# Kernel optimization log

Hardware: AMD Instinct MI355X
Metric: run time of the kernel (lower is better)

## Reference

```python
import jax, jax.numpy as jnp
import numpy as np

NUM_HEADS = 16


def setup_inputs() -> dict:
    key = jax.random.key(0)
    ks = jax.random.split(key, 5)
    B, S, E = 4, 2048, 1024
    scale = 1.0 / np.sqrt(E)
    return {
        "x": jax.random.normal(ks[0], (B, S, E), dtype=jnp.float32),
        "w_in": jax.random.normal(ks[1], (E, 3 * E), dtype=jnp.float32) * scale,
        "b_in": jax.random.normal(ks[2], (3 * E,), dtype=jnp.float32) * 0.02,
        "w_out": jax.random.normal(ks[3], (E, E), dtype=jnp.float32) * scale,
        "b_out": jax.random.normal(ks[4], (E,), dtype=jnp.float32) * 0.02,
    }


def reference(x, w_in, b_in, w_out, b_out):
    B, S, E = x.shape
    H = NUM_HEADS
    D = E // H  # head dim
    qkv = x @ w_in + b_in                      # [B,S,3E]
    q, k, v = jnp.split(qkv, 3, axis=-1)       # each [B,S,E]
    q = q.reshape(B, S, H, D)
    k = k.reshape(B, S, H, D)
    v = v.reshape(B, S, H, D)
    # scores scaled by 1/sqrt(D); note: original's causal masked_fill is a
    # no-op (not in-place), so attention is unmasked.
    scores = jnp.einsum("bqhd,bkhd->bhqk", q, k) / jnp.sqrt(jnp.float32(D))
    attn = jax.nn.softmax(scores, axis=-1)      # [B,H,S,S]
    out = jnp.einsum("bhqk,bkhd->bqhd", attn, v).reshape(B, S, E)
    return out @ w_out + b_out
```

## Files before the change

### kernel.cpp

```cpp
#include <hip/hip_runtime.h>
#include <math.h>

#define B_ 4
#define S_ 2048
#define E_ 1024
#define H_ 16
#define D_ 64
#define M_ (B_ * S_)

using f32x4  = __attribute__((ext_vector_type(4))) float;
using short8 = __attribute__((ext_vector_type(8))) short;
using half8  = __attribute__((ext_vector_type(8))) _Float16;
using ushort8_t = __attribute__((ext_vector_type(8))) unsigned short;

__device__ inline unsigned short f2h(float f) {
    _Float16 h = (_Float16)f;
    unsigned short u; __builtin_memcpy(&u, &h, 2); return u;
}
__device__ inline unsigned pk2h(float a, float b) {
    auto t = __builtin_amdgcn_cvt_pkrtz(a, b);
    unsigned u; __builtin_memcpy(&u, &t, 4); return u;
}
__device__ inline float ex2(float x) {
#if __has_builtin(__builtin_amdgcn_exp2f)
    return __builtin_amdgcn_exp2f(x);
#else
    return exp2f(x);
#endif
}
__device__ inline f32x4 mfma16(short8 a, short8 b, f32x4 c) {
    half8 ha, hb;
    __builtin_memcpy(&ha, &a, 16);
    __builtin_memcpy(&hb, &b, 16);
    return __builtin_amdgcn_mfma_f32_16x16x32_f16(ha, hb, c, 0, 0, 0);
}
__device__ inline void gload_lds16(const void* g, void* l) {
    __builtin_amdgcn_global_load_lds(
        (const __attribute__((address_space(1))) void*)g,
        (__attribute__((address_space(3))) void*)l, 16, 0, 0);
}

#define QSCALE 0.18033688f

__global__ __launch_bounds__(256)
void prep_kernel(const float* __restrict__ x,     unsigned short* __restrict__ xh,
                 const float* __restrict__ w_in,  unsigned short* __restrict__ wInTh,
                 const float* __restrict__ w_out, unsigned short* __restrict__ wOutTh)
{
    __shared__ float t[32][33];
    const int bid  = blockIdx.x;
    const int tidx = threadIdx.x;
    if (bid < (M_ * E_) / 1024) {
        const size_t i = ((size_t)bid * 256 + tidx) * 4;
        float4 v = *(const float4*)(x + i);
        ushort4 hh;
        hh.x = f2h(v.x); hh.y = f2h(v.y); hh.z = f2h(v.z); hh.w = f2h(v.w);
        *(ushort4*)(xh + i) = hh;
        return;
    }
    const float* W; unsigned short* T; int C, c0, r0;
    if (bid < 8192 + 3072) {
        const int t2 = bid - 8192;
        W = w_in;  T = wInTh;  C = 3 * E_;
        c0 = (t2 % 96) * 32;  r0 = (t2 / 96) * 32;
    } else {
        const int t2 = bid - 11264;
        W = w_out; T = wOutTh; C = E_;
        c0 = (t2 & 31) * 32;  r0 = (t2 >> 5) * 32;
    }
    const int tx = tidx & 31, ty = tidx >> 5;
    #pragma unroll
    for (int i = 0; i < 4; ++i)
        t[ty + 8 * i][tx] = W[(size_t)(r0 + ty + 8 * i) * C + c0 + tx];
    __syncthreads();
    #pragma unroll
    for (int i = 0; i < 4; ++i)
        T[(size_t)(c0 + ty + 8 * i) * E_ + r0 + tx] = f2h(t[tx][ty + 8 * i]);
}

template<int OUT_MODE>
__global__ __launch_bounds__(256)
void gemm_mfma_kernel(const unsigned short* __restrict__ Ah,
                      const unsigned short* __restrict__ Bt,
                      const float* __restrict__ bias,
                      float* __restrict__ Cf,
                      unsigned short* __restrict__ Ch,
                      int M, int N, int K)
{
    __shared__ unsigned short As[128][64];
    __shared__ unsigned short Bs[128][64];

    const int tid  = threadIdx.x;
    const int lane = tid & 63;
    const int wave = tid >> 6;
    const int wm = (wave >> 1) * 64, wn = (wave & 1) * 64;
    const int ln = lane & 15, qd = lane >> 4;
    const int m0 = blockIdx.x * 128, n0 = blockIdx.y * 128;

    f32x4 acc[4][4] = {};

    const int srow_l = lane >> 3;
    const int scol   = ((lane & 7) ^ srow_l) * 8;
    const int swz    = (ln & 7) * 8;

    for (int k0 = 0; k0 < K; k0 += 64) {
        #pragma unroll
        for (int c = 0; c < 4; ++c) {
            const int r = wave * 32 + c * 8;
            const size_t ga = (size_t)(m0 + r + srow_l) * K + k0 + scol;
            const size_t gb = (size_t)(n0 + r + srow_l) * K + k0 + scol;
            gload_lds16(Ah + ga, &As[r][0]);
            gload_lds16(Bt + gb, &Bs[r][0]);
        }
        __syncthreads();

        #pragma unroll
        for (int ks = 0; ks < 2; ++ks) {
            const int co = (ks * 32 + qd * 8) ^ swz;
            short8 aa[4], bb[4];
            #pragma unroll
            for (int mt = 0; mt < 4; ++mt)
                aa[mt] = *(const short8*)&As[wm + mt * 16 + ln][co];
            #pragma unroll
            for (int nt = 0; nt < 4; ++nt)
                bb[nt] = *(const short8*)&Bs[wn + nt * 16 + ln][co];
            __builtin_amdgcn_s_setprio(1);
            #pragma unroll
            for (int mt = 0; mt < 4; ++mt)
                #pragma unroll
                for (int nt = 0; nt < 4; ++nt)
                    acc[mt][nt] = mfma16(aa[mt], bb[nt], acc[mt][nt]);
            __builtin_amdgcn_s_setprio(0);
        }
        __syncthreads();
    }

    #pragma unroll
    for (int nt = 0; nt < 4; ++nt) {
        const int col = n0 + wn + nt * 16 + ln;
        const float bv = bias[col];
        const float scale = (OUT_MODE == 2 && col < E_) ? QSCALE : 1.0f;
        #pragma unroll
        for (int mt = 0; mt < 4; ++mt) {
            #pragma unroll
            for (int r = 0; r < 4; ++r) {
                const int row = m0 + wm + mt * 16 + qd * 4 + r;
                float f = acc[mt][nt][r] + bv;
                size_t idx = (size_t)row * N + col;
                if (OUT_MODE == 0) Cf[idx] = f;
                else               Ch[idx] = f2h(f * scale);
            }
        }
    }
}

__global__ __launch_bounds__(512)
void attn_mfma_kernel(const unsigned short* __restrict__ qkvh,
                      unsigned short* __restrict__ outh)
{
    constexpr int TQ = 256, TK = 64, LD = 64;
    __shared__ unsigned short Ksh[TK][LD];
    __shared__ unsigned short VthA[D_][LD];
    __shared__ unsigned short VthB[D_][LD];

    const int tid  = threadIdx.x;
    const int lane = tid & 63;
    const int wave = tid >> 6;
    const int ln = lane & 15, qd = lane >> 4;
    const int id   = blockIdx.x;
    const int g    = id & 63;
    const int qblk = id >> 6;
    const int h    = g & 15;
    const int b    = g >> 4;
    const int wq0 = wave * 32;
    const int swz = (ln & 7) * 8;

    short8 ones8;
    #pragma unroll
    for (int j = 0; j < 8; ++j) ones8[j] = (short)0x3C00;

    short8 qh[2][2];
    #pragma unroll
    for (int qt = 0; qt < 2; ++qt)
        #pragma unroll
        for (int ks = 0; ks < 2; ++ks) {
            size_t base = ((size_t)(b * S_ + qblk * TQ + wq0 + qt * 16 + ln)) * (3 * E_)
                        + h * 64 + ks * 32 + qd * 8;
            qh[qt][ks] = *(const short8*)(qkvh + base);
        }

    f32x4 o[4][2] = {};
    f32x4 ol[2]   = {};
    short8 pBp[2][2] = {};

    const int stid = tid & 255;
    const int krow = stid >> 2, kcol = (stid & 3) * 16;
    const int kswz = (krow & 7) * 8;
    const int vkey = (stid & 31) * 2, vdc = (stid >> 5) * 8;
    const int vslot = (vkey & 0x23) | ((vkey & 0x0C) << 1) | ((vkey & 0x10) >> 2);

    {
        ushort8_t z = {};
        *(ushort8_t*)(&VthB[0][0] + tid * 8) = z;
    }

    ushort8_t pk0 = {}, pk1 = {}, pv0 = {}, pv1 = {};
    if (wave < 4) {
        size_t gb = ((size_t)(b * S_ + krow)) * (3 * E_) + E_ + h * 64 + kcol;
        pk0 = *(const ushort8_t*)(qkvh + gb);
        pk1 = *(const ushort8_t*)(qkvh + gb + 8);
    } else {
        size_t vb0 = ((size_t)(b * S_ + vkey)) * (3 * E_) + 2 * E_ + h * 64 + vdc;
        pv0 = *(const ushort8_t*)(qkvh + vb0);
        pv1 = *(const ushort8_t*)(qkvh + vb0 + 3 * E_);
    }

    #define TILE_BODY(VW, VR, PREFETCH_KB, DO_PREFETCH)                        \
    {                                                                          \
        if (wave < 4) {                                                        \
            *(ushort8_t*)&Ksh[krow][kcol ^ kswz]       = pk0;                  \
            *(ushort8_t*)&Ksh[krow][(kcol + 8) ^ kswz] = pk1;                  \
        } else {                                                               \
            _Pragma("unroll")                                                  \
            for (int j = 0; j < 8; ++j)                                        \
                *(unsigned*)&VW[vdc + j][vslot ^ (j * 8)] =                    \
                    (unsigned)pv0[j] | ((unsigned)pv1[j] << 16);               \
        }                                                                      \
        __syncthreads();                                                       \
        if (DO_PREFETCH) {                                                     \
            if (wave < 4) {                                                    \
                size_t gb_ = ((size_t)(b * S_ + (PREFETCH_KB) + krow))         \
                           * (3 * E_) + E_ + h * 64 + kcol;                    \
                pk0 = *(const ushort8_t*)(qkvh + gb_);                         \
                pk1 = *(const ushort8_t*)(qkvh + gb_ + 8);                     \
            } else {                                                           \
                size_t vb_ = ((size_t)(b * S_ + (PREFETCH_KB) + vkey))         \
                           * (3 * E_) + 2 * E_ + h * 64 + vdc;                 \
                pv0 = *(const ushort8_t*)(qkvh + vb_);                         \
                pv1 = *(const ushort8_t*)(qkvh + vb_ + 3 * E_);                \
            }                                                                  \
        }                                                                      \
        f32x4 st[4][2] = {};                                                   \
        _Pragma("unroll")                                                      \
        for (int ks = 0; ks < 2; ++ks) {                                       \
            const int co = (ks * 32 + qd * 8) ^ swz;                           \
            short8 kh[4];                                                      \
            _Pragma("unroll")                                                  \
            for (int kt = 0; kt < 4; ++kt)                                     \
                kh[kt] = *(const short8*)&Ksh[kt * 16 + ln][co];               \
            __builtin_amdgcn_s_setprio(1);                                     \
            _Pragma("unroll")                                                  \
            for (int kt = 0; kt < 4; ++kt)                                     \
                _Pragma("unroll")                                              \
                for (int qt = 0; qt < 2; ++qt)                                 \
                    st[kt][qt] = mfma16(kh[kt], qh[qt][ks], st[kt][qt]);       \
            __builtin_amdgcn_s_setprio(0);                                     \
        }                                                                      \
                \
        _Pragma("unroll")                                                      \
        for (int ks = 0; ks < 2; ++ks) {                                       \
            const int co = (ks * 32 + qd * 8) ^ swz;                           \
            short8 vA[4];                                                      \
            _Pragma("unroll")                                                  \
            for (int dt = 0; dt < 4; ++dt)                                     \
                vA[dt] = *(const short8*)&VR[dt * 16 + ln][co];                \
            __builtin_amdgcn_s_setprio(1);                                     \
            _Pragma("unroll")                                                  \
            for (int dt = 0; dt < 4; ++dt)                                     \
                _Pragma("unroll")                                              \
                for (int qt = 0; qt < 2; ++qt)                                 \
                    o[dt][qt] = mfma16(vA[dt], pBp[ks][qt], o[dt][qt]);        \
            _Pragma("unroll")                                                  \
            for (int qt = 0; qt < 2; ++qt)                                     \
                ol[qt] = mfma16(ones8, pBp[ks][qt], ol[qt]);                   \
            __builtin_amdgcn_s_setprio(0);                                     \
        }                                                                      \
                             \
        _Pragma("unroll")                                                      \
        for (int qt = 0; qt < 2; ++qt)                                         \
            _Pragma("unroll")                                                  \
            for (int ks = 0; ks < 2; ++ks) {                                   \
                unsigned w_[4];                                                \
                w_[0] = pk2h(ex2(st[2 * ks][qt][0]), ex2(st[2 * ks][qt][1]));  \
                w_[1] = pk2h(ex2(st[2 * ks][qt][2]), ex2(st[2 * ks][qt][3]));  \
                w_[2] = pk2h(ex2(st[2 * ks + 1][qt][0]),                       \
                             ex2(st[2 * ks + 1][qt][1]));                      \
                w_[3] = pk2h(ex2(st[2 * ks + 1][qt][2]),                       \
                             ex2(st[2 * ks + 1][qt][3]));                      \
                __builtin_memcpy(&pBp[ks][qt], w_, 16);                        \
            }                                                                  \
        __syncthreads();                                                       \
    }

    for (int kb = 0; kb < S_; kb += 2 * TK) {
        TILE_BODY(VthA, VthB, kb + TK, true);
        TILE_BODY(VthB, VthA, kb + 2 * TK, (kb + 2 * TK < S_));
    }
    #undef TILE_BODY

    #pragma unroll
    for (int ks = 0; ks < 2; ++ks) {
        const int co = (ks * 32 + qd * 8) ^ swz;
        short8 vA[4];
        #pragma unroll
        for (int dt = 0; dt < 4; ++dt)
            vA[dt] = *(const short8*)&VthB[dt * 16 + ln][co];
        #pragma unroll
        for (int dt = 0; dt < 4; ++dt)
            #pragma unroll
            for (int qt = 0; qt < 2; ++qt)
                o[dt][qt] = mfma16(vA[dt], pBp[ks][qt], o[dt][qt]);
        #pragma unroll
        for (int qt = 0; qt < 2; ++qt)
            ol[qt] = mfma16(ones8, pBp[ks][qt], ol[qt]);
    }

    float inv[2];
    #pragma unroll
    for (int qt = 0; qt < 2; ++qt)
        inv[qt] = 1.0f / ol[qt][0];
    #pragma unroll
    for (int qt = 0; qt < 2; ++qt) {
        const int q = qblk * TQ + wq0 + qt * 16 + ln;
        #pragma unroll
        for (int dt = 0; dt < 4; ++dt) {
            size_t base = ((size_t)(b * S_ + q)) * E_ + h * 64 + dt * 16 + qd * 4;
            ushort4 hh;
            #pragma unroll
            for (int r = 0; r < 4; ++r)
                ((unsigned short*)&hh)[r] = f2h(o[dt][qt][r] * inv[qt]);
            *(ushort4*)(outh + base) = hh;
        }
    }
}

extern "C" void kernel_launch(void* const* d_in, const int* in_sizes, int n_in,
                              void* d_out, int out_size, void* d_ws, size_t ws_size,
                              hipStream_t stream)
{
    const float* x     = (const float*)d_in[0];
    const float* w_in  = (const float*)d_in[1];
    const float* b_in  = (const float*)d_in[2];
    const float* w_out = (const float*)d_in[3];
    const float* b_out = (const float*)d_in[4];
    float* outp = (float*)d_out;

    char* ws = (char*)d_ws;
    unsigned short* qkvh   = (unsigned short*)ws;
    unsigned short* attnh  = qkvh   + (size_t)M_ * 3 * E_;
    unsigned short* xh     = attnh  + (size_t)M_ * E_;
    unsigned short* wOutTh = xh     + (size_t)M_ * E_;
    unsigned short* wInTh  = attnh;

    prep_kernel<<<dim3(8192 + 3072 + 1024), 256, 0, stream>>>(
        x, xh, w_in, wInTh, w_out, wOutTh);

    gemm_mfma_kernel<2><<<dim3(M_ / 128, (3 * E_) / 128), 256, 0, stream>>>(
        xh, wInTh, b_in, nullptr, qkvh, M_, 3 * E_, E_);

    attn_mfma_kernel<<<dim3((S_ / 256) * H_ * B_), 512, 0, stream>>>(
        qkvh, attnh);

    gemm_mfma_kernel<0><<<dim3(M_ / 128, E_ / 128), 256, 0, stream>>>(
        attnh, wOutTh, b_out, outp, nullptr, M_, E_, E_);
}
```

Before: 267.8 us.

## Double-buffer LDS tiles in MFMA GEMM to overlap global loads with compute

The GEMM kernel now keeps two LDS buffers for the A and B tiles and issues the global-to-LDS loads for the next K tile before computing on the current one. Explicit vmcnt waits let the prefetch stay in flight while the current tile is consumed. This hides global load latency behind MFMA work in the QKV and output projections. In exchange, LDS use per block doubles to 64KB, which may lower occupancy, and correctness depends on the hand-written waitcnt counts matching the number of outstanding loads.

```diff
diff --git a/kernel.cpp b/kernel.cpp
--- a/kernel.cpp
+++ b/kernel.cpp
@@ -87,8 +87,8 @@
                       unsigned short* __restrict__ Ch,
                       int M, int N, int K)
 {
-    __shared__ unsigned short As[128][64];
-    __shared__ unsigned short Bs[128][64];
+    __shared__ unsigned short As[2][128][64];
+    __shared__ unsigned short Bs[2][128][64];
 
     const int tid  = threadIdx.x;
     const int lane = tid & 63;
@@ -103,16 +103,31 @@
     const int scol   = ((lane & 7) ^ srow_l) * 8;
     const int swz    = (ln & 7) * 8;
 
-    for (int k0 = 0; k0 < K; k0 += 64) {
-        #pragma unroll
-        for (int c = 0; c < 4; ++c) {
-            const int r = wave * 32 + c * 8;
-            const size_t ga = (size_t)(m0 + r + srow_l) * K + k0 + scol;
-            const size_t gb = (size_t)(n0 + r + srow_l) * K + k0 + scol;
-            gload_lds16(Ah + ga, &As[r][0]);
-            gload_lds16(Bt + gb, &Bs[r][0]);
-        }
-        __syncthreads();
+    #pragma unroll
+    for (int c = 0; c < 4; ++c) {
+        const int r = wave * 32 + c * 8;
+        gload_lds16(Ah + (size_t)(m0 + r + srow_l) * K + scol, &As[0][r][0]);
+        gload_lds16(Bt + (size_t)(n0 + r + srow_l) * K + scol, &Bs[0][r][0]);
+    }
+
+    const int NT = K >> 6;
+    int cur = 0;
+    for (int t = 0; t < NT; ++t) {
+        if (t + 1 < NT) {
+            const int k1 = (t + 1) << 6;
+            #pragma unroll
+            for (int c = 0; c < 4; ++c) {
+                const int r = wave * 32 + c * 8;
+                gload_lds16(Ah + (size_t)(m0 + r + srow_l) * K + k1 + scol,
+                            &As[cur ^ 1][r][0]);
+                gload_lds16(Bt + (size_t)(n0 + r + srow_l) * K + k1 + scol,
+                            &Bs[cur ^ 1][r][0]);
+            }
+            asm volatile("s_waitcnt vmcnt(8)" ::: "memory");
+        } else {
+            asm volatile("s_waitcnt vmcnt(0)" ::: "memory");
+        }
+        __builtin_amdgcn_s_barrier();
 
         #pragma unroll
         for (int ks = 0; ks < 2; ++ks) {
@@ -120,10 +135,10 @@
             short8 aa[4], bb[4];
             #pragma unroll
             for (int mt = 0; mt < 4; ++mt)
-                aa[mt] = *(const short8*)&As[wm + mt * 16 + ln][co];
+                aa[mt] = *(const short8*)&As[cur][wm + mt * 16 + ln][co];
             #pragma unroll
             for (int nt = 0; nt < 4; ++nt)
-                bb[nt] = *(const short8*)&Bs[wn + nt * 16 + ln][co];
+                bb[nt] = *(const short8*)&Bs[cur][wn + nt * 16 + ln][co];
             __builtin_amdgcn_s_setprio(1);
             #pragma unroll
             for (int mt = 0; mt < 4; ++mt)
@@ -132,7 +147,9 @@
                     acc[mt][nt] = mfma16(aa[mt], bb[nt], acc[mt][nt]);
             __builtin_amdgcn_s_setprio(0);
         }
-        __syncthreads();
+        asm volatile("s_waitcnt lgkmcnt(0)" ::: "memory");
+        __builtin_amdgcn_s_barrier();
+        cur ^= 1;
     }
 
     #pragma unroll
```

After: 261.1 us. 1.03x faster.
